# Performance work log

Hardware: AMD Instinct MI355X
Metric: run time of the kernel (lower is better)

## Reference

```python
import jax, jax.numpy as jnp
import numpy as np

RATIO = 0.25
K = 32
LN_EPS = 1e-5


def _fps(xyz, npoint):
    """Farthest point sampling. xyz [B,N,3] -> idx [B,npoint] (int32).
    Deterministic start at index 0 (torch version uses randint)."""
    B, N, _ = xyz.shape
    init_dist = jnp.full((B, N), 1e10, dtype=xyz.dtype)
    init_far = jnp.zeros((B,), dtype=jnp.int32)

    def step(carry, _):
        dist, far = carry
        centroid = jnp.take_along_axis(xyz, far[:, None, None], axis=1)  # [B,1,3]
        d = jnp.sum((xyz - centroid) ** 2, axis=-1)                      # [B,N]
        dist = jnp.minimum(dist, d)
        new_far = jnp.argmax(dist, axis=-1).astype(jnp.int32)
        return (dist, new_far), far  # emit the index BEFORE update (matches torch)

    _, idx = jax.lax.scan(step, (init_dist, init_far), None, length=npoint)
    return idx.T  # [B,npoint]


def _knn(x, k):
    """k-nearest neighbors by squared distance. x [B,S,3] -> idx [B,S,k]."""
    xx = jnp.sum(x ** 2, axis=-1, keepdims=True)            # [B,S,1]
    inner = jnp.einsum('bsd,btd->bst', x, x)                # [B,S,S]
    neg_sqdist = 2.0 * inner - xx - jnp.swapaxes(xx, 1, 2)  # -||xi-xj||^2
    return jax.lax.top_k(neg_sqdist, k)[1]                  # [B,S,k]


def _gather(pts, idx):
    """pts [B,N,C], idx [B,...] -> [B,...,C]."""
    B = pts.shape[0]
    flat = idx.reshape(B, -1)
    out = jnp.take_along_axis(pts, flat[..., None], axis=1)
    return out.reshape(idx.shape + (pts.shape[-1],))


def _forward(xyz, features, W1, b1, gamma, beta, W2, b2):
    B, N, _ = xyz.shape
    npoint = max(int(N * RATIO), 1)
    k = min(K, N)

    fps_idx = _fps(xyz, npoint)                 # [B,S]
    new_xyz = _gather(xyz, fps_idx)             # [B,S,3]

    # NOTE: module computes knn(xyz) + gathers but never uses them (dead code) -> skipped.
    # Faithful quirk: knn over new_xyz gives indices in [0,npoint) which the
    # original then uses to index the ORIGINAL xyz/features.
    fps_nb_idx = _knn(new_xyz, min(K, N))       # [B,S,k]
    nb_xyz = _gather(xyz, fps_nb_idx)           # [B,S,k,3]
    nb_feat = _gather(features, fps_nb_idx)     # [B,S,k,C]

    pos_diff = nb_xyz - new_xyz[:, :, None, :]
    combined = jnp.concatenate([nb_feat, pos_diff], axis=-1)  # [B,S,k,C+3]

    h = combined @ W1 + b1                      # [B,S,k,O]
    mu = jnp.mean(h, axis=-1, keepdims=True)
    var = jnp.var(h, axis=-1, keepdims=True)
    h = (h - mu) * jax.lax.rsqrt(var + LN_EPS) * gamma + beta
    h = jax.nn.relu(h)
    h = h @ W2 + b2
    new_features = jnp.max(h, axis=2)           # [B,S,O]
    return new_xyz, new_features


def setup_inputs() -> dict:
    key = jax.random.key(0)
    ks = jax.random.split(key, 4)
    B, N, C, O = 4, 16384, 64, 128
    xyz = jax.random.normal(ks[0], (B, N, 3), dtype=jnp.float32)
    features = jax.random.normal(ks[1], (B, N, C), dtype=jnp.float32)
    W1 = jax.random.normal(ks[2], (C + 3, O), dtype=jnp.float32) * 0.05
    b1 = jnp.zeros((O,), jnp.float32)
    gamma = jnp.ones((O,), jnp.float32)
    beta = jnp.zeros((O,), jnp.float32)
    W2 = jax.random.normal(ks[3], (O, O), dtype=jnp.float32) * 0.05
    b2 = jnp.zeros((O,), jnp.float32)
    return {"xyz": xyz, "features": features, "W1": W1, "b1": b1,
            "gamma": gamma, "beta": beta, "W2": W2, "b2": b2}


def reference(xyz, features, W1, b1, gamma, beta, W2, b2):
    return _forward(xyz, features, W1, b1, gamma, beta, W2, b2)
```

## Files before the change

kernel.cpp:

```cpp
#include <hip/hip_runtime.h>
#include <cstdint>

typedef unsigned long long ull;

#define B_ 4
#define N_ 16384
#define C_ 64
#define O_ 128
#define S_ 4096
#define K_ 32
#define CK_ 67

__device__ __forceinline__ unsigned part3_4(unsigned v) {
  return (v & 1u) | ((v & 2u) << 2) | ((v & 4u) << 4) | ((v & 8u) << 6);
}

__launch_bounds__(1024, 1)
__global__ void sort_kernel(const float* __restrict__ xyz,
                            float4* __restrict__ sorted) {
  const int b = blockIdx.x, t = threadIdx.x;
  const int lane = t & 63, wid = t >> 6;
  __shared__ unsigned hist[4096];
  __shared__ unsigned wsum[16];
  for (int i = t; i < 4096; i += 1024) hist[i] = 0u;
  __syncthreads();
  const float* base = xyz + (size_t)b * N_ * 3;
  int cell[16];
#pragma unroll
  for (int j = 0; j < 16; ++j) {
    int p = j * 1024 + t;
    float x = base[p * 3 + 0], y = base[p * 3 + 1], z = base[p * 3 + 2];
    int cx = (int)floorf((x + 6.0f) * (16.0f / 12.0f));
    int cy = (int)floorf((y + 6.0f) * (16.0f / 12.0f));
    int cz = (int)floorf((z + 6.0f) * (16.0f / 12.0f));
    cx = min(max(cx, 0), 15); cy = min(max(cy, 0), 15); cz = min(max(cz, 0), 15);
    int m = (int)(part3_4((unsigned)cx) | (part3_4((unsigned)cy) << 1) |
                  (part3_4((unsigned)cz) << 2));
    cell[j] = m;
    atomicAdd(&hist[m], 1u);
  }
  __syncthreads();
  unsigned h0 = hist[4 * t + 0], h1 = hist[4 * t + 1];
  unsigned h2 = hist[4 * t + 2], h3 = hist[4 * t + 3];
  unsigned s4 = h0 + h1 + h2 + h3;
  unsigned inc = s4;
#pragma unroll
  for (int off = 1; off < 64; off <<= 1) {
    unsigned n = __shfl_up(inc, off);
    if (lane >= off) inc += n;
  }
  if (lane == 63) wsum[wid] = inc;
  __syncthreads();
  if (t < 16) {
    unsigned v = wsum[t], iv = v;
#pragma unroll
    for (int off = 1; off < 16; off <<= 1) {
      unsigned n = __shfl_up(iv, off);
      if (t >= off) iv += n;
    }
    wsum[t] = iv - v;
  }
  __syncthreads();
  unsigned st = wsum[wid] + (inc - s4);
  hist[4 * t + 0] = st;
  hist[4 * t + 1] = st + h0;
  hist[4 * t + 2] = st + h0 + h1;
  hist[4 * t + 3] = st + h0 + h1 + h2;
  __syncthreads();
#pragma unroll
  for (int j = 0; j < 16; ++j) {
    int p = j * 1024 + t;
    float x = base[p * 3 + 0], y = base[p * 3 + 1], z = base[p * 3 + 2];
    unsigned pos = atomicAdd(&hist[cell[j]], 1u);
    float4 o;
    o.x = x; o.y = y; o.z = z; o.w = __uint_as_float((unsigned)p);
    sorted[(size_t)b * N_ + pos] = o;
  }
}

__launch_bounds__(512, 1)
__global__ void fps_kernel(const float* __restrict__ xyz,
                           const float4* __restrict__ sorted,
                           float* __restrict__ new_xyz) {
#pragma clang fp contract(off)
  const int b = blockIdx.x, t = threadIdx.x;
  const int lane = t & 63, wid = t >> 6;
  const float4* sb = sorted + (size_t)b * N_;
  __shared__ float lds_dist[N_];
  __shared__ float aabb[256][6];
  __shared__ ull regmax[256];
  __shared__ unsigned short list_[256];
  __shared__ unsigned cnt[2];
  __shared__ ull s_wbest[8];

  for (int i = t; i < N_; i += 512) lds_dist[i] = 1e10f;
  const ull INITKEY = ((ull)__float_as_uint(1e10f)) << 28;
  for (int r = t; r < 256; r += 512) regmax[r] = INITKEY;
  if (t == 0) { cnt[0] = 0u; cnt[1] = 0u; }
  for (int r = wid; r < 256; r += 8) {
    float4 v = sb[r * 64 + lane];
    float lx = v.x, hx = v.x, ly = v.y, hy = v.y, lz = v.z, hz = v.z;
#pragma unroll
    for (int off = 1; off < 64; off <<= 1) {
      lx = fminf(lx, __shfl_xor(lx, off)); hx = fmaxf(hx, __shfl_xor(hx, off));
      ly = fminf(ly, __shfl_xor(ly, off)); hy = fmaxf(hy, __shfl_xor(hy, off));
      lz = fminf(lz, __shfl_xor(lz, off)); hz = fmaxf(hz, __shfl_xor(hz, off));
    }
    if (lane == 0) {
      aabb[r][0] = lx; aabb[r][1] = hx; aabb[r][2] = ly;
      aabb[r][3] = hy; aabb[r][4] = lz; aabb[r][5] = hz;
    }
  }
  const float* ob = xyz + (size_t)b * N_ * 3;
  float fx = ob[0], fy = ob[1], fz = ob[2];
  __syncthreads();

  for (int s = 0; s < S_; ++s) {
    const int buf = s & 1;
    if (t == 0) {
      float* o = new_xyz + ((size_t)b * S_ + s) * 3;
      o[0] = fx; o[1] = fy; o[2] = fz;
      cnt[buf ^ 1] = 0u;
    }
    if (t < 256) {
      float dxm = fmaxf(fmaxf(aabb[t][0] - fx, fx - aabb[t][1]), 0.0f);
      float dym = fmaxf(fmaxf(aabb[t][2] - fy, fy - aabb[t][3]), 0.0f);
      float dzm = fmaxf(fmaxf(aabb[t][4] - fz, fz - aabb[t][5]), 0.0f);
      float lb = dxm * dxm + dym * dym + dzm * dzm;
      float bmax = __uint_as_float((unsigned)(regmax[t] >> 28));
      if (lb * 0.99998f < bmax) {
        unsigned idx = atomicAdd(&cnt[buf], 1u);
        list_[idx] = (unsigned short)t;
      }
    }
    __syncthreads();
    const int nneed = (int)cnt[buf];
    for (int p = 0; p < nneed; p += 8) {
      const int li = p + wid;
      if (li < nneed) {
        const int r = list_[li];
        float4 v = sb[r * 64 + lane];
        float dx = v.x - fx;
        float dy = v.y - fy;
        float dz = v.z - fz;
        float d = dx * dx + dy * dy + dz * dz;
        const int pi = r * 64 + lane;
        float m = fminf(lds_dist[pi], d);
        lds_dist[pi] = m;
        unsigned og = __float_as_uint(v.w);
        ull key = (((ull)__float_as_uint(m)) << 28) |
                  (((ull)((~og) & 0x3FFFu)) << 14) | (unsigned)pi;
#pragma unroll
        for (int off = 1; off < 64; off <<= 1) {
          ull o = __shfl_xor(key, off);
          if (o > key) key = o;
        }
        if (lane == 0) regmax[r] = key;
      }
    }
    __syncthreads();
    ull k = 0;
    if (lane < 32) k = regmax[wid * 32 + lane];
#pragma unroll
    for (int off = 1; off < 64; off <<= 1) {
      ull o = __shfl_xor(k, off);
      if (o > k) k = o;
    }
    if (lane == 0) s_wbest[wid] = k;
    __syncthreads();
    ull kb = s_wbest[0];
#pragma unroll
    for (int w = 1; w < 8; ++w) {
      ull o = s_wbest[w];
      if (o > kb) kb = o;
    }
    float4 c = sb[(unsigned)(kb & 0x3FFFu)];
    fx = c.x; fy = c.y; fz = c.z;
  }
}

__launch_bounds__(256, 2)
__global__ void knn_kernel(const float* __restrict__ new_xyz,
                           int* __restrict__ knn_idx) {
  const int b = blockIdx.y;
  const int t = threadIdx.x;
  const int q = blockIdx.x * 256 + t;
  __shared__ float sx[S_], sy[S_], sz[S_], sn[S_];
  const float* nb = new_xyz + (size_t)b * S_ * 3;
  for (int i = t; i < S_; i += 256) {
    float x = nb[i * 3 + 0], y = nb[i * 3 + 1], z = nb[i * 3 + 2];
    sx[i] = x; sy[i] = y; sz[i] = z;
    sn[i] = fmaf(z, z, fmaf(y, y, x * x));
  }
  __syncthreads();
  const float qx = sx[q], qy = sy[q], qz = sz[q], qn = sn[q];
  unsigned long long kv[K_];
#pragma unroll
  for (int j = 0; j < K_; ++j) kv[j] = 0ull;
  for (int i = 0; i < S_; ++i) {
    float inner = fmaf(sz[i], qz, fmaf(sy[i], qy, sx[i] * qx));
    float score = (2.0f * inner - qn) - sn[i];
    unsigned u = __float_as_uint(score);
    u ^= (unsigned)((int)u >> 31) | 0x80000000u;
    unsigned long long nk = ((unsigned long long)u << 32) | (unsigned)(~i);
    if (nk > kv[K_ - 1]) {
#pragma unroll
      for (int j = K_ - 1; j >= 1; --j) {
        bool upPrev = nk > kv[j - 1];
        kv[j] = upPrev ? kv[j - 1] : ((nk > kv[j]) ? nk : kv[j]);
      }
      if (nk > kv[0]) kv[0] = nk;
    }
  }
#pragma unroll
  for (int j = 0; j < K_; ++j)
    knn_idx[((size_t)b * S_ + q) * K_ + j] = (int)(~(unsigned)kv[j]);
}

#define W1S 76
#define W2S 132
#define CLS 72
#define HPS 132

__launch_bounds__(256, 1)
__global__ void mlp_kernel(const float* __restrict__ xyz,
                           const float* __restrict__ features,
                           const float* __restrict__ new_xyz,
                           const int* __restrict__ knn_idx,
                           const float* __restrict__ W1,
                           const float* __restrict__ b1,
                           const float* __restrict__ gamma,
                           const float* __restrict__ beta,
                           const float* __restrict__ W2,
                           const float* __restrict__ b2,
                           float* __restrict__ out_feat) {
  __shared__ float w1T[O_][W1S];
  __shared__ float w2T[O_][W2S];
  __shared__ float c_l[K_][CLS];
  __shared__ float hp[K_][HPS];
  __shared__ float pmaxl[8][O_];

  const int t = threadIdx.x;
  const int g = t >> 5;
  const int cg = t & 31;

  for (int e = t; e < CK_ * O_; e += 256) {
    int k = e >> 7, c = e & (O_ - 1);
    w1T[c][k] = W1[e];
  }
  if (t < O_) {
#pragma unroll
    for (int k = CK_; k < 68; ++k) w1T[t][k] = 0.0f;
  }
  for (int e = t; e < O_ * O_; e += 256) {
    int k = e >> 7, c = e & (O_ - 1);
    w2T[c][k] = W2[e];
  }
  float bb1[4], gm[4], bt[4], bb2 = 0.0f;
#pragma unroll
  for (int j = 0; j < 4; ++j) {
    bb1[j] = b1[cg + 32 * j];
    gm[j] = gamma[cg + 32 * j];
    bt[j] = beta[cg + 32 * j];
  }
  if (t < O_) bb2 = b2[t];

  const int bs0 = blockIdx.x * 64;
  const int b = bs0 >> 12;
  const float* fb = features + (size_t)b * N_ * C_;
  const float* xb = xyz + (size_t)b * N_ * 3;

  __syncthreads();

  for (int is = 0; is < 64; ++is) {
    const int bs = bs0 + is;
    const float qx = new_xyz[(size_t)bs * 3 + 0];
    const float qy = new_xyz[(size_t)bs * 3 + 1];
    const float qz = new_xyz[(size_t)bs * 3 + 2];

    for (int e = t; e < K_ * 68; e += 256) {
      int r = e / 68;
      int k = e - r * 68;
      int nbi = knn_idx[(size_t)bs * K_ + r];
      float v;
      if (k < C_) {
        v = fb[(size_t)nbi * C_ + k];
      } else if (k < CK_) {
        float coord = xb[nbi * 3 + (k - C_)];
        float qq = (k == C_) ? qx : ((k == C_ + 1) ? qy : qz);
        v = coord - qq;
      } else {
        v = 0.0f;
      }
      c_l[r][k] = v;
    }
    __syncthreads();

    float h[4][4];
#pragma unroll
    for (int i = 0; i < 4; ++i)
#pragma unroll
      for (int j = 0; j < 4; ++j) h[i][j] = 0.0f;
#pragma unroll
    for (int kc = 0; kc < 17; ++kc) {
      float4 w[4], a[4];
#pragma unroll
      for (int j = 0; j < 4; ++j)
        w[j] = *reinterpret_cast<const float4*>(&w1T[cg + 32 * j][kc * 4]);
#pragma unroll
      for (int i = 0; i < 4; ++i)
        a[i] = *reinterpret_cast<const float4*>(&c_l[4 * g + i][kc * 4]);
#pragma unroll
      for (int i = 0; i < 4; ++i)
#pragma unroll
        for (int j = 0; j < 4; ++j) {
          h[i][j] = fmaf(a[i].x, w[j].x, h[i][j]);
          h[i][j] = fmaf(a[i].y, w[j].y, h[i][j]);
          h[i][j] = fmaf(a[i].z, w[j].z, h[i][j]);
          h[i][j] = fmaf(a[i].w, w[j].w, h[i][j]);
        }
    }
#pragma unroll
    for (int i = 0; i < 4; ++i)
#pragma unroll
      for (int j = 0; j < 4; ++j) h[i][j] += bb1[j];

#pragma unroll
    for (int i = 0; i < 4; ++i) {
      float s1 = (h[i][0] + h[i][1]) + (h[i][2] + h[i][3]);
      float s2 = ((h[i][0] * h[i][0] + h[i][1] * h[i][1]) +
                  (h[i][2] * h[i][2] + h[i][3] * h[i][3]));
#pragma unroll
      for (int off = 1; off <= 16; off <<= 1) {
        s1 += __shfl_xor(s1, off);
        s2 += __shfl_xor(s2, off);
      }
      float mu = s1 * (1.0f / 128.0f);
      float va = fmaf(mu, -mu, s2 * (1.0f / 128.0f));
      float rs = rsqrtf(va + 1e-5f);
#pragma unroll
      for (int j = 0; j < 4; ++j) {
        float hv = fmaf((h[i][j] - mu) * rs, gm[j], bt[j]);
        hp[4 * g + i][cg + 32 * j] = fmaxf(hv, 0.0f);
      }
    }
    __syncthreads();

    float acc[4][4];
#pragma unroll
    for (int i = 0; i < 4; ++i)
#pragma unroll
      for (int j = 0; j < 4; ++j) acc[i][j] = 0.0f;
#pragma unroll 8
    for (int kc = 0; kc < 32; ++kc) {
      float4 w[4], a[4];
#pragma unroll
      for (int j = 0; j < 4; ++j)
        w[j] = *reinterpret_cast<const float4*>(&w2T[cg + 32 * j][kc * 4]);
#pragma unroll
      for (int i = 0; i < 4; ++i)
        a[i] = *reinterpret_cast<const float4*>(&hp[4 * g + i][kc * 4]);
#pragma unroll
      for (int i = 0; i < 4; ++i)
#pragma unroll
        for (int j = 0; j < 4; ++j) {
          acc[i][j] = fmaf(a[i].x, w[j].x, acc[i][j]);
          acc[i][j] = fmaf(a[i].y, w[j].y, acc[i][j]);
          acc[i][j] = fmaf(a[i].z, w[j].z, acc[i][j]);
          acc[i][j] = fmaf(a[i].w, w[j].w, acc[i][j]);
        }
    }
#pragma unroll
    for (int j = 0; j < 4; ++j) {
      float pm = fmaxf(fmaxf(acc[0][j], acc[1][j]), fmaxf(acc[2][j], acc[3][j]));
      pmaxl[g][cg + 32 * j] = pm;
    }
    __syncthreads();

    if (t < O_) {
      float m = pmaxl[0][t];
#pragma unroll
      for (int w = 1; w < 8; ++w) m = fmaxf(m, pmaxl[w][t]);
      out_feat[(size_t)bs * O_ + t] = m + bb2;
    }
    __syncthreads();
  }
}

extern "C" void kernel_launch(void* const* d_in, const int* in_sizes, int n_in,
                              void* d_out, int out_size, void* d_ws, size_t ws_size,
                              hipStream_t stream) {
  const float* xyz      = (const float*)d_in[0];
  const float* features = (const float*)d_in[1];
  const float* W1       = (const float*)d_in[2];
  const float* b1       = (const float*)d_in[3];
  const float* gamma    = (const float*)d_in[4];
  const float* beta     = (const float*)d_in[5];
  const float* W2       = (const float*)d_in[6];
  const float* b2       = (const float*)d_in[7];

  float* out      = (float*)d_out;
  float* new_xyz  = out;
  float* new_feat = out + (size_t)B_ * S_ * 3;
  int* knn_idx = (int*)d_ws;
  float4* sorted = (float4*)((char*)d_ws + (size_t)B_ * S_ * K_ * 4);

  sort_kernel<<<B_, 1024, 0, stream>>>(xyz, sorted);
  fps_kernel<<<B_, 512, 0, stream>>>(xyz, sorted, new_xyz);
  knn_kernel<<<dim3(S_ / 256, B_), 256, 0, stream>>>(new_xyz, knn_idx);
  mlp_kernel<<<B_ * S_ / 64, 256, 0, stream>>>(xyz, features, new_xyz, knn_idx,
                                               W1, b1, gamma, beta, W2, b2,
                                               new_feat);
}
```

Measured before the change: 11.00 ms.

## Keep FPS region bounds and maxima in wave registers, cut per-step barriers

Each wave now owns a fixed set of 32 spatial regions. Region bounding boxes and per-region max keys sit in lane registers instead of shared memory, and the region work list is built with a wave ballot instead of a shared atomic counter. This removes one of the two block-wide barriers per FPS iteration and the shared-memory traffic for aabb, regmax and the list. The shared best-per-wave array is double-buffered to avoid a write-after-read hazard. The key no longer stores the sorted position, so the next centroid is fetched from the original xyz by index. Work is now fixed per wave, so the load can become uneven when the regions that need updating are concentrated in a few waves.

```diff
diff --git a/kernel.cpp b/kernel.cpp
--- a/kernel.cpp
+++ b/kernel.cpp
@@ -87,17 +87,13 @@
   const int lane = t & 63, wid = t >> 6;
   const float4* sb = sorted + (size_t)b * N_;
   __shared__ float lds_dist[N_];
-  __shared__ float aabb[256][6];
-  __shared__ ull regmax[256];
-  __shared__ unsigned short list_[256];
-  __shared__ unsigned cnt[2];
-  __shared__ ull s_wbest[8];
+  __shared__ ull s_wavebest[2][8];
 
   for (int i = t; i < N_; i += 512) lds_dist[i] = 1e10f;
-  const ull INITKEY = ((ull)__float_as_uint(1e10f)) << 28;
-  for (int r = t; r < 256; r += 512) regmax[r] = INITKEY;
-  if (t == 0) { cnt[0] = 0u; cnt[1] = 0u; }
-  for (int r = wid; r < 256; r += 8) {
+
+  float alox = 0.f, ahix = 0.f, aloy = 0.f, ahiy = 0.f, aloz = 0.f, ahiz = 0.f;
+  for (int rl = 0; rl < 32; ++rl) {
+    const int r = (wid << 5) + rl;
     float4 v = sb[r * 64 + lane];
     float lx = v.x, hx = v.x, ly = v.y, hy = v.y, lz = v.z, hz = v.z;
 #pragma unroll
@@ -106,13 +102,15 @@
       ly = fminf(ly, __shfl_xor(ly, off)); hy = fmaxf(hy, __shfl_xor(hy, off));
       lz = fminf(lz, __shfl_xor(lz, off)); hz = fmaxf(hz, __shfl_xor(hz, off));
     }
-    if (lane == 0) {
-      aabb[r][0] = lx; aabb[r][1] = hx; aabb[r][2] = ly;
-      aabb[r][3] = hy; aabb[r][4] = lz; aabb[r][5] = hz;
-    }
-  }
+    if (lane == rl) {
+      alox = lx; ahix = hx; aloy = ly; ahiy = hy; aloz = lz; ahiz = hz;
+    }
+  }
+
   const float* ob = xyz + (size_t)b * N_ * 3;
   float fx = ob[0], fy = ob[1], fz = ob[2];
+  ull regkey = ((ull)__float_as_uint(1e10f)) << 14;
+  ull wbest = 0;
   __syncthreads();
 
   for (int s = 0; s < S_; ++s) {
@@ -120,25 +118,22 @@
     if (t == 0) {
       float* o = new_xyz + ((size_t)b * S_ + s) * 3;
       o[0] = fx; o[1] = fy; o[2] = fz;
-      cnt[buf ^ 1] = 0u;
-    }
-    if (t < 256) {
-      float dxm = fmaxf(fmaxf(aabb[t][0] - fx, fx - aabb[t][1]), 0.0f);
-      float dym = fmaxf(fmaxf(aabb[t][2] - fy, fy - aabb[t][3]), 0.0f);
-      float dzm = fmaxf(fmaxf(aabb[t][4] - fz, fz - aabb[t][5]), 0.0f);
+    }
+    bool need = false;
+    if (lane < 32) {
+      float dxm = fmaxf(fmaxf(alox - fx, fx - ahix), 0.0f);
+      float dym = fmaxf(fmaxf(aloy - fy, fy - ahiy), 0.0f);
+      float dzm = fmaxf(fmaxf(aloz - fz, fz - ahiz), 0.0f);
       float lb = dxm * dxm + dym * dym + dzm * dzm;
-      float bmax = __uint_as_float((unsigned)(regmax[t] >> 28));
-      if (lb * 0.99998f < bmax) {
-        unsigned idx = atomicAdd(&cnt[buf], 1u);
-        list_[idx] = (unsigned short)t;
-      }
-    }
-    __syncthreads();
-    const int nneed = (int)cnt[buf];
-    for (int p = 0; p < nneed; p += 8) {
-      const int li = p + wid;
-      if (li < nneed) {
-        const int r = list_[li];
+      float bmax = __uint_as_float((unsigned)(regkey >> 14));
+      need = (lb * 0.99998f < bmax);
+    }
+    ull mask = __ballot(need);
+    if (mask) {
+      do {
+        const int rl = (int)(__ffsll(mask) - 1);
+        mask &= mask - 1;
+        const int r = (wid << 5) + rl;
         float4 v = sb[r * 64 + lane];
         float dx = v.x - fx;
         float dy = v.y - fy;
@@ -148,34 +143,32 @@
         float m = fminf(lds_dist[pi], d);
         lds_dist[pi] = m;
         unsigned og = __float_as_uint(v.w);
-        ull key = (((ull)__float_as_uint(m)) << 28) |
-                  (((ull)((~og) & 0x3FFFu)) << 14) | (unsigned)pi;
+        ull key = (((ull)__float_as_uint(m)) << 14) | ((~og) & 0x3FFFu);
 #pragma unroll
         for (int off = 1; off < 64; off <<= 1) {
           ull o = __shfl_xor(key, off);
           if (o > key) key = o;
         }
-        if (lane == 0) regmax[r] = key;
+        if (lane == rl) regkey = key;
+      } while (mask);
+      ull k = (lane < 32) ? regkey : 0ull;
+#pragma unroll
+      for (int off = 1; off < 64; off <<= 1) {
+        ull o = __shfl_xor(k, off);
+        if (o > k) k = o;
       }
-    }
+      wbest = k;
+    }
+    if (lane == 0) s_wavebest[buf][wid] = wbest;
     __syncthreads();
-    ull k = 0;
-    if (lane < 32) k = regmax[wid * 32 + lane];
-#pragma unroll
-    for (int off = 1; off < 64; off <<= 1) {
-      ull o = __shfl_xor(k, off);
-      if (o > k) k = o;
-    }
-    if (lane == 0) s_wbest[wid] = k;
-    __syncthreads();
-    ull kb = s_wbest[0];
+    ull kb = s_wavebest[buf][0];
 #pragma unroll
     for (int w = 1; w < 8; ++w) {
-      ull o = s_wbest[w];
+      ull o = s_wavebest[buf][w];
       if (o > kb) kb = o;
     }
-    float4 c = sb[(unsigned)(kb & 0x3FFFu)];
-    fx = c.x; fy = c.y; fz = c.z;
+    const unsigned og = (~(unsigned)kb) & 0x3FFFu;
+    fx = ob[og * 3 + 0]; fy = ob[og * 3 + 1]; fz = ob[og * 3 + 2];
   }
 }
 
```

Measured after the change: 18.87 ms. 71.5% more time.
